# Optimization experiments

Hardware: AMD Instinct MI355X
Metric: run time of the kernel (lower is better)

## Reference

```python
import jax, jax.numpy as jnp
import numpy as np

B, T, N, D, FF = 4, 288, 207, 152, 256  # batch, time, nodes, model_dim, feed_forward_dim


def setup_inputs() -> dict:
    key = jax.random.key(0)
    k0, k1, k2 = jax.random.split(key, 3)
    X = jax.random.normal(k0, (B, T, N, D), dtype=jnp.float32)
    Wq = jax.random.normal(k1, (FF, N * D), dtype=jnp.float32) * 0.02
    bq = jnp.zeros((FF,), jnp.float32)
    Wk = jax.random.normal(k2, (FF, N * D), dtype=jnp.float32) * 0.02
    bk = jnp.zeros((FF,), jnp.float32)
    return {"X": X, "Wq": Wq, "bq": bq, "Wk": Wk, "bk": bk, "K": 6}


def reference(X, Wq, bq, Wk, bk, K):
    b, t, n, d = X.shape
    x_pack = X.reshape(b, t, n * d)                      # (B,T,N*D)
    q = x_pack @ Wq.T + bq                               # (B,T,FF)
    k = x_pack @ Wk.T + bk                               # (B,T,FF)
    q_fft = jnp.fft.rfft(q, axis=-1)                     # (B,T,FF//2+1) complex
    k_fft = jnp.fft.rfft(k, axis=-1)
    # cross-correlation in frequency domain: (B,T,T,F)
    cross_fft = q_fft[:, :, None, :] * jnp.conj(k_fft)[:, None, :, :]
    # NOTE: original uses ifft (not irfft) over the rfft-length axis, takes real part
    cross_corr = jnp.fft.ifft(cross_fft, axis=-1).real   # (B,T,T,F)
    corr_matrix = cross_corr.mean(axis=-1).mean(axis=0)  # (T,T)
    corr_matrix = jnp.where(jnp.eye(t, dtype=bool), -jnp.inf, corr_matrix)
    topk_values, topk_indices = jax.lax.top_k(corr_matrix, K)   # (T,K), descending values
    order = jnp.argsort(topk_indices, axis=-1)                  # ascending index order
    sorted_values = jnp.take_along_axis(topk_values, order, axis=-1)   # (T,K)
    sorted_indices = jnp.take_along_axis(topk_indices, order, axis=-1)  # (T,K)
    # gather X at selected timesteps: (B,T,K,N,D) == X[b, sorted_indices[t,k], n, d]
    sorted_values_from_X = X[:, sorted_indices]          # (B,T,K,N,D)
    return sorted_values, sorted_indices, sorted_values_from_X
```

## Files before the change

### kernel.cpp

```cpp
#include <hip/hip_runtime.h>
#include <math.h>

#define B_  4
#define T_  288
#define N_  207
#define D_  152
#define FF_ 256
#define ND_ (N_*D_)
#define ND4 (ND_/4)
#define K_  6
#define CH_ 8
#define CHSZ 984

typedef float vfloat4 __attribute__((ext_vector_type(4)));

__global__ void colsum_kernel(const float* __restrict__ Wq,
                              const float* __restrict__ Wk,
                              float* __restrict__ wq_sum,
                              float* __restrict__ wk_sum) {
    int j = blockIdx.x * blockDim.x + threadIdx.x;
    if (j >= ND4) return;
    const vfloat4* W  = (const vfloat4*)((blockIdx.y == 0) ? Wq : Wk);
    vfloat4*      out = (vfloat4*)((blockIdx.y == 0) ? wq_sum : wk_sum);
    vfloat4 s = {0.f, 0.f, 0.f, 0.f};
    #pragma unroll 4
    for (int ff = 0; ff < FF_; ++ff)
        s += __builtin_nontemporal_load(&W[(size_t)ff * ND4 + j]);
    out[j] = s;
}

__global__ void biassum_kernel(const float* __restrict__ bq,
                               const float* __restrict__ bk,
                               float* __restrict__ bsum) {
    __shared__ float shq[256], shk[256];
    int tid = threadIdx.x;
    shq[tid] = bq[tid];
    shk[tid] = bk[tid];
    __syncthreads();
    for (int s = 128; s > 0; s >>= 1) {
        if (tid < s) { shq[tid] += shq[tid + s]; shk[tid] += shk[tid + s]; }
        __syncthreads();
    }
    if (tid == 0) { bsum[0] = shq[0]; bsum[1] = shk[0]; }
}

__global__ void rowdot_kernel(const float* __restrict__ X,
                              const float* __restrict__ wq_sum,
                              const float* __restrict__ wk_sum,
                              const float* __restrict__ bsum,
                              float* __restrict__ sq,
                              float* __restrict__ sk,
                              int*   __restrict__ cnt) {
    int row = blockIdx.x;
    int tid = threadIdx.x;
    if (row < T_ && tid == 0) cnt[row] = 0;
    const vfloat4* x4 = (const vfloat4*)(X + (size_t)row * ND_);
    const vfloat4* q4 = (const vfloat4*)wq_sum;
    const vfloat4* k4 = (const vfloat4*)wk_sum;
    float pq = 0.f, pk = 0.f;
    for (int j = tid; j < ND4; j += 256) {
        vfloat4 xv = x4[j];
        vfloat4 qv = q4[j];
        vfloat4 kv = k4[j];
        pq += xv.x*qv.x + xv.y*qv.y + xv.z*qv.z + xv.w*qv.w;
        pk += xv.x*kv.x + xv.y*kv.y + xv.z*kv.z + xv.w*kv.w;
    }
    __shared__ float shq[256], shk[256];
    shq[tid] = pq; shk[tid] = pk;
    __syncthreads();
    for (int s = 128; s > 0; s >>= 1) {
        if (tid < s) { shq[tid] += shq[tid + s]; shk[tid] += shk[tid + s]; }
        __syncthreads();
    }
    if (tid == 0) {
        sq[row] = shq[0] + bsum[0];
        sk[row] = shk[0] + bsum[1];
    }
}

#define SLOTS 5
__global__ __launch_bounds__(64) void topk_kernel(
                            const float* __restrict__ sq,
                            const float* __restrict__ sk,
                            float* __restrict__ out_vals,
                            float* __restrict__ out_idx_f,
                            int*   __restrict__ cnt,
                            int*   __restrict__ lists) {
    int t1   = blockIdx.x;
    int lane = threadIdx.x;
    float sq0 = sq[0*T_ + t1], sq1 = sq[1*T_ + t1];
    float sq2 = sq[2*T_ + t1], sq3 = sq[3*T_ + t1];

    float v[SLOTS]; int vi[SLOTS];
    #pragma unroll
    for (int s = 0; s < SLOTS; ++s) {
        int t2 = lane + s * 64;
        if (t2 < T_ && t2 != t1) {
            float c = sq0*sk[0*T_ + t2] + sq1*sk[1*T_ + t2]
                    + sq2*sk[2*T_ + t2] + sq3*sk[3*T_ + t2];
            v[s]  = c * (1.0f / (129.0f * (float)B_));
            vi[s] = t2;
        } else {
            v[s]  = -INFINITY;
            vi[s] = 0x7fffffff;
        }
    }

    float tv[K_]; int ti[K_];
    for (int k = 0; k < K_; ++k) {
        float bv = v[0]; int bi = vi[0];
        #pragma unroll
        for (int s = 1; s < SLOTS; ++s) {
            if (v[s] > bv || (v[s] == bv && vi[s] < bi)) { bv = v[s]; bi = vi[s]; }
        }
        #pragma unroll
        for (int off = 32; off > 0; off >>= 1) {
            float ov = __shfl_xor(bv, off);
            int   oi = __shfl_xor(bi, off);
            if (ov > bv || (ov == bv && oi < bi)) { bv = ov; bi = oi; }
        }
        tv[k] = bv; ti[k] = bi;
        #pragma unroll
        for (int s = 0; s < SLOTS; ++s)
            if (vi[s] == bi) { v[s] = -INFINITY; vi[s] = 0x7fffffff; }
    }

    if (lane == 0) {
        for (int a = 1; a < K_; ++a) {
            float vv = tv[a]; int ii = ti[a]; int b = a - 1;
            while (b >= 0 && ti[b] > ii) { tv[b+1] = tv[b]; ti[b+1] = ti[b]; --b; }
            tv[b+1] = vv; ti[b+1] = ii;
        }
        for (int k = 0; k < K_; ++k) {
            out_vals [t1*K_ + k] = tv[k];
            out_idx_f[t1*K_ + k] = (float)ti[k];
            int src = ti[k];
            int pos = atomicAdd(&cnt[src], 1);
            lists[src * T_ + pos] = t1 * K_ + k;
        }
    }
}

__global__ __launch_bounds__(256) void gather_kernel(
                              const float* __restrict__ X,
                              const int* __restrict__ cnt,
                              const int* __restrict__ lists,
                              float* __restrict__ out3) {
    int c   = blockIdx.x;
    int src = blockIdx.y;
    int b   = blockIdx.z;
    int n = cnt[src];
    if (n == 0) return;
    const int j0 = c * CHSZ;
    const int j1 = (j0 + CHSZ < ND4) ? (j0 + CHSZ) : ND4;
    const vfloat4* srcp = (const vfloat4*)(X + ((size_t)b * T_ + src) * ND_);
    const int* lst = lists + src * T_;

    vfloat4 r[4];
    #pragma unroll
    for (int u = 0; u < 4; ++u) {
        int j = j0 + (int)threadIdx.x + u * 256;
        if (j < j1) r[u] = srcp[j];
    }
    for (int e = 0; e < n; ++e) {
        int rk = lst[e];
        vfloat4* dst = (vfloat4*)(out3 + ((size_t)b * (T_ * K_) + rk) * ND_);
        #pragma unroll
        for (int u = 0; u < 4; ++u) {
            int j = j0 + (int)threadIdx.x + u * 256;
            if (j < j1) dst[j] = r[u];
        }
    }
}

extern "C" void kernel_launch(void* const* d_in, const int* in_sizes, int n_in,
                              void* d_out, int out_size, void* d_ws, size_t ws_size,
                              hipStream_t stream) {
    const float* X  = (const float*)d_in[0];
    const float* Wq = (const float*)d_in[1];
    const float* bq = (const float*)d_in[2];
    const float* Wk = (const float*)d_in[3];
    const float* bk = (const float*)d_in[4];

    float* ws = (float*)d_ws;
    float* wq_sum = ws;
    float* wk_sum = ws + ND_;
    float* bsum   = ws + 2*ND_;
    float* sq     = ws + 2*ND_ + 4;
    float* sk     = sq + B_*T_;
    int*   cnt    = (int*)(sk + B_*T_);
    int*   lists  = cnt + T_;

    float* out_vals  = (float*)d_out;
    float* out_idx_f = out_vals + T_*K_;
    float* out3      = out_idx_f + T_*K_;

    dim3 g1((ND4 + 255)/256, 2);
    colsum_kernel<<<g1, 256, 0, stream>>>(Wq, Wk, wq_sum, wk_sum);
    biassum_kernel<<<1, 256, 0, stream>>>(bq, bk, bsum);
    rowdot_kernel<<<B_*T_, 256, 0, stream>>>(X, wq_sum, wk_sum, bsum, sq, sk, cnt);
    topk_kernel<<<T_, 64, 0, stream>>>(sq, sk, out_vals, out_idx_f, cnt, lists);
    gather_kernel<<<dim3(CH_, T_, B_), 256, 0, stream>>>(X, cnt, lists, out3);
}
```

Before: 314.9 us.

## Flatten gather into one block per output row via compacted source ordering

Adds an order kernel that prefix-sums per-source counts and builds a compact list of (destination row, source timestep) pairs, sorted by source. The gather then launches one block per output row and batch, streaming the whole source row with nontemporal stores. This replaces the old chunked per-source blocks, which loaded each source slice once and wrote it n times. The aim is to remove idle blocks for unused sources and the imbalance from varying fan-out, at the cost of rereading a source row from memory or cache for every destination and an extra serial single-block launch.

```diff
diff --git a/kernel.cpp b/kernel.cpp
--- a/kernel.cpp
+++ b/kernel.cpp
@@ -9,8 +9,7 @@
 #define ND_ (N_*D_)
 #define ND4 (ND_/4)
 #define K_  6
-#define CH_ 8
-#define CHSZ 984
+#define TK_ (T_*K_)
 
 typedef float vfloat4 __attribute__((ext_vector_type(4)));
 
@@ -141,35 +140,43 @@
     }
 }
 
+__global__ __launch_bounds__(320) void order_kernel(
+                            const int* __restrict__ cnt,
+                            const int* __restrict__ lists,
+                            int* __restrict__ prefix,
+                            int* __restrict__ order,
+                            int* __restrict__ srcof) {
+    int tid = threadIdx.x;
+    if (tid == 0) {
+        int acc = 0;
+        for (int s = 0; s < T_; ++s) { prefix[s] = acc; acc += cnt[s]; }
+        prefix[T_] = acc;
+    }
+    __syncthreads();
+    if (tid < T_) {
+        int base = prefix[tid];
+        int n    = cnt[tid];
+        for (int e = 0; e < n; ++e) {
+            order[base + e] = lists[tid * T_ + e];
+            srcof[base + e] = tid;
+        }
+    }
+}
+
 __global__ __launch_bounds__(256) void gather_kernel(
                               const float* __restrict__ X,
-                              const int* __restrict__ cnt,
-                              const int* __restrict__ lists,
+                              const int* __restrict__ order,
+                              const int* __restrict__ srcof,
                               float* __restrict__ out3) {
-    int c   = blockIdx.x;
-    int src = blockIdx.y;
-    int b   = blockIdx.z;
-    int n = cnt[src];
-    if (n == 0) return;
-    const int j0 = c * CHSZ;
-    const int j1 = (j0 + CHSZ < ND4) ? (j0 + CHSZ) : ND4;
+    int p = blockIdx.x;
+    int b = blockIdx.y;
+    int rk  = order[p];
+    int src = srcof[p];
     const vfloat4* srcp = (const vfloat4*)(X + ((size_t)b * T_ + src) * ND_);
-    const int* lst = lists + src * T_;
-
-    vfloat4 r[4];
-    #pragma unroll
-    for (int u = 0; u < 4; ++u) {
-        int j = j0 + (int)threadIdx.x + u * 256;
-        if (j < j1) r[u] = srcp[j];
-    }
-    for (int e = 0; e < n; ++e) {
-        int rk = lst[e];
-        vfloat4* dst = (vfloat4*)(out3 + ((size_t)b * (T_ * K_) + rk) * ND_);
-        #pragma unroll
-        for (int u = 0; u < 4; ++u) {
-            int j = j0 + (int)threadIdx.x + u * 256;
-            if (j < j1) dst[j] = r[u];
-        }
+    vfloat4*       dst  = (vfloat4*)(out3 + ((size_t)b * TK_ + rk) * ND_);
+    for (int j = threadIdx.x; j < ND4; j += 256) {
+        vfloat4 val = srcp[j];
+        __builtin_nontemporal_store(val, &dst[j]);
     }
 }
 
@@ -190,15 +197,19 @@
     float* sk     = sq + B_*T_;
     int*   cnt    = (int*)(sk + B_*T_);
     int*   lists  = cnt + T_;
+    int*   prefix = lists + T_*T_;
+    int*   order  = prefix + T_ + 1;
+    int*   srcof  = order + TK_;
 
     float* out_vals  = (float*)d_out;
-    float* out_idx_f = out_vals + T_*K_;
-    float* out3      = out_idx_f + T_*K_;
+    float* out_idx_f = out_vals + TK_;
+    float* out3      = out_idx_f + TK_;
 
     dim3 g1((ND4 + 255)/256, 2);
     colsum_kernel<<<g1, 256, 0, stream>>>(Wq, Wk, wq_sum, wk_sum);
     biassum_kernel<<<1, 256, 0, stream>>>(bq, bk, bsum);
     rowdot_kernel<<<B_*T_, 256, 0, stream>>>(X, wq_sum, wk_sum, bsum, sq, sk, cnt);
     topk_kernel<<<T_, 64, 0, stream>>>(sq, sk, out_vals, out_idx_f, cnt, lists);
-    gather_kernel<<<dim3(CH_, T_, B_), 256, 0, stream>>>(X, cnt, lists, out3);
-}
+    order_kernel<<<1, 320, 0, stream>>>(cnt, lists, prefix, order, srcof);
+    gather_kernel<<<dim3(TK_, B_), 256, 0, stream>>>(X, order, srcof, out3);
+}
```

Measured after the change: 305.5 us. 1.03x faster.
